# Performance work log

Measured on AMD Instinct MI355X. Metric: run time of the kernel, lower is better.

The kernel has to match this reference:

```python
import jax, jax.numpy as jnp
import numpy as np

N = 100000
E = 1600000
F_IN = 128
F_OUT = 200


def setup_inputs() -> dict:
    key = jax.random.key(0)
    ks = jax.random.split(key, 10)
    x = jax.random.normal(ks[0], (N, F_IN), dtype=jnp.float32)
    edge_index = jax.random.randint(ks[1], (2, E), 0, N, dtype=jnp.int64)
    edge_weight = jax.random.uniform(ks[2], (E,), dtype=jnp.float32)
    s = 1.0 / np.sqrt(F_IN)
    W1 = jax.random.uniform(ks[3], (1, F_IN, F_OUT), dtype=jnp.float32, minval=-s, maxval=s)
    b1 = jnp.zeros((F_OUT,), dtype=jnp.float32)
    W2 = jax.random.uniform(ks[4], (2, F_IN, F_OUT), dtype=jnp.float32, minval=-s, maxval=s)
    b2 = jnp.zeros((F_OUT,), dtype=jnp.float32)
    W3 = jax.random.uniform(ks[5], (3, F_IN, F_OUT), dtype=jnp.float32, minval=-s, maxval=s)
    b3 = jnp.zeros((F_OUT,), dtype=jnp.float32)
    return {"x": x, "edge_index": edge_index, "edge_weight": edge_weight,
            "W1": W1, "b1": b1, "W2": W2, "b2": b2, "W3": W3, "b3": b3}


def _cheb_norm(edge_index, edge_weight, n):
    # PyG ChebConv norm with lambda_max=2.0: scaled Laplacian L_hat = L - I
    # off-diagonal entries: -w_ij * d_i^{-1/2} * d_j^{-1/2}; diagonal: 0
    row, col = edge_index[0], edge_index[1]
    deg = jax.ops.segment_sum(edge_weight, row, num_segments=n)
    dis = jnp.where(deg > 0, jax.lax.rsqrt(jnp.where(deg > 0, deg, 1.0)), 0.0)
    return -edge_weight * dis[row] * dis[col]


def _propagate(h, row, col, norm, n):
    # h: [N, F] -> sum over incoming edges of norm_e * h[col_e]
    return jax.ops.segment_sum(norm[:, None] * h[col], row, num_segments=n)


def _chebconv(x, row, col, norm, W, b, n):
    K = W.shape[0]
    Tx_prev2 = x
    out = jnp.einsum('nf,fo->no', x, W[0])
    if K > 1:
        Tx_prev = _propagate(x, row, col, norm, n)
        out = out + jnp.einsum('nf,fo->no', Tx_prev, W[1])
        for k in range(2, K):
            Tx_k = 2.0 * _propagate(Tx_prev, row, col, norm, n) - Tx_prev2
            out = out + jnp.einsum('nf,fo->no', Tx_k, W[k])
            Tx_prev2, Tx_prev = Tx_prev, Tx_k
    return out + b


def reference(x, edge_index, edge_weight, W1, b1, W2, b2, W3, b3):
    n = x.shape[0]
    row, col = edge_index[0], edge_index[1]
    norm = _cheb_norm(edge_index, edge_weight, n)
    scale_1 = _chebconv(x, row, col, norm, W1, b1, n)
    scale_2 = _chebconv(x, row, col, norm, W2, b2, n)
    scale_3 = _chebconv(x, row, col, norm, W3, b3, n)
    return (scale_1, scale_2, scale_3)
```

## Files before the change

kernel.cpp:

```cpp
#include <hip/hip_runtime.h>
#include <hip/hip_bf16.h>
#include <stdint.h>

#define NN    100000
#define NROWP 100096
#define NE    1600000
#define FIN   128
#define FOUT  200
#define NBLK  391

typedef __attribute__((ext_vector_type(8))) short short8;
typedef __attribute__((ext_vector_type(8))) unsigned short ushort8;
typedef __attribute__((ext_vector_type(2))) float f32x2;
typedef __attribute__((ext_vector_type(4))) float f32x4;
typedef __attribute__((ext_vector_type(2))) unsigned int u32x2;
typedef __attribute__((ext_vector_type(4))) unsigned int uint32x4;

__device__ __forceinline__ short f2bf(float f) {
    __hip_bfloat16 h = __float2bfloat16(f);
    return *reinterpret_cast<short*>(&h);
}
__device__ __forceinline__ unsigned short f2bfu(float f) {
    __hip_bfloat16 h = __float2bfloat16(f);
    return *reinterpret_cast<unsigned short*>(&h);
}
__device__ __forceinline__ float bf2f(unsigned short u) {
    return __uint_as_float((unsigned)u << 16);
}
__device__ __forceinline__ int getidx(const void* ei, int isI32, long long i) {
    return isI32 ? ((const int*)ei)[i] : (int)((const long long*)ei)[i];
}

__global__ void detect_kernel(const long long* ei64, int* flag) {
    int t = blockIdx.x * blockDim.x + threadIdx.x;
    long long v = ei64[t];
    if (v < 0 || v >= NN) atomicOr(flag, 1);
}

__global__ void cnt8_kernel(const void* ei, const int* flag, int* cnt8) {
    int e = blockIdx.x * blockDim.x + threadIdx.x;
    int r = getidx(ei, *flag, e);
    atomicAdd(&cnt8[(blockIdx.x & 7) * NN + r], 1);
}

__global__ void scan_block(int* __restrict__ cnt8, int* __restrict__ rowstart,
                           int* __restrict__ bsum) {
    __shared__ int tmp[256];
    int i = blockIdx.x * 256 + threadIdx.x;
    int v = 0;
    if (i < NN) {
        int s = 0;
        #pragma unroll
        for (int x = 0; x < 8; ++x) {
            int c = cnt8[x * NN + i];
            cnt8[x * NN + i] = s;
            s += c;
        }
        v = s;
    }
    tmp[threadIdx.x] = v;
    __syncthreads();
    for (int off = 1; off < 256; off <<= 1) {
        int t = (threadIdx.x >= off) ? tmp[threadIdx.x - off] : 0;
        __syncthreads();
        tmp[threadIdx.x] += t;
        __syncthreads();
    }
    if (i < NN) rowstart[i] = tmp[threadIdx.x] - v;
    if (threadIdx.x == 255) bsum[blockIdx.x] = tmp[255];
}

__global__ void scan_bsums(int* bsum) {
    __shared__ int tmp[512];
    int t = threadIdx.x;
    int v = (t < NBLK) ? bsum[t] : 0;
    tmp[t] = v;
    __syncthreads();
    for (int off = 1; off < 512; off <<= 1) {
        int u = (t >= off) ? tmp[t - off] : 0;
        __syncthreads();
        tmp[t] += u;
        __syncthreads();
    }
    if (t < NBLK) bsum[t] = tmp[t] - v;
}

__global__ void scan_add(int* __restrict__ rowstart, const int* __restrict__ bsum) {
    int i = blockIdx.x * 256 + threadIdx.x;
    if (i < NN)       rowstart[i] += bsum[i >> 8];
    else if (i == NN) rowstart[NN] = NE;
}

__global__ void fill_csr(const void* ei, const int* flag, const float* __restrict__ w,
                         const int* __restrict__ rowstart, int* __restrict__ cnt8,
                         int2* __restrict__ edge) {
    int e = blockIdx.x * blockDim.x + threadIdx.x;
    int isI32 = *flag;
    int r = getidx(ei, isI32, e);
    int c = getidx(ei, isI32, (long long)NE + e);
    int pos = rowstart[r] + atomicAdd(&cnt8[(blockIdx.x & 7) * NN + r], 1);
    int2 rec; rec.x = c; rec.y = __float_as_int(w[e]);
    edge[pos] = rec;
}

__global__ void deg_seg(const int* __restrict__ rowstart, const int2* __restrict__ edge,
                        float* __restrict__ dis) {
    int r = blockIdx.x * 256 + threadIdx.x;
    if (r >= NN) return;
    int s = rowstart[r], e = rowstart[r + 1];
    float d = 0.f;
    for (int i = s; i < e; ++i) d += __int_as_float(edge[i].y);
    dis[r] = d > 0.f ? rsqrtf(d) : 0.f;
}

__global__ void xconv_kernel(const float* __restrict__ x, const float* __restrict__ dis,
                             unsigned short* __restrict__ xb, unsigned int* __restrict__ xs8) {
    int i = blockIdx.x * 256 + threadIdx.x;
    float d = dis[i >> 4];
    long long base = (long long)i * 8;
    f32x4 v0 = *(const f32x4*)(x + base);
    f32x4 v1 = *(const f32x4*)(x + base + 4);
    ushort8 o;
    #pragma unroll
    for (int k = 0; k < 4; ++k) { o[k] = f2bfu(v0[k]); o[4 + k] = f2bfu(v1[k]); }
    __builtin_nontemporal_store(o, (ushort8*)(xb + base));
    unsigned u0 = __builtin_amdgcn_cvt_pk_fp8_f32(d * v0[0], d * v0[1], 0, false);
    u0 = __builtin_amdgcn_cvt_pk_fp8_f32(d * v0[2], d * v0[3], u0, true);
    unsigned u1 = __builtin_amdgcn_cvt_pk_fp8_f32(d * v1[0], d * v1[1], 0, false);
    u1 = __builtin_amdgcn_cvt_pk_fp8_f32(d * v1[2], d * v1[3], u1, true);
    u32x2 ov; ov[0] = u0; ov[1] = u1;
    __builtin_nontemporal_store(ov, (u32x2*)(xs8 + (long long)i * 2));
}

template <int MODE>
__launch_bounds__(256)
__global__ void gather_prop(const int* __restrict__ rowstart, const int2* __restrict__ edge,
                            const float* __restrict__ dis,
                            const unsigned int* __restrict__ src8,
                            const unsigned short* __restrict__ xb,
                            unsigned short* __restrict__ dstb,
                            unsigned int* __restrict__ dst8) {
    int gw   = (blockIdx.x << 2) + (threadIdx.x >> 6);
    int lane = threadIdx.x & 63;
    int q = lane >> 4, fl = lane & 15;
    int s = rowstart[gw], eend = rowstart[gw + 1];
    float a0[8] = {0.f,0.f,0.f,0.f,0.f,0.f,0.f,0.f};
    float a1[8] = {0.f,0.f,0.f,0.f,0.f,0.f,0.f,0.f};
    int e = s + q;
    for (; e + 4 < eend; e += 8) {
        int2 ed0 = edge[e];
        int2 ed1 = edge[e + 4];
        u32x2 v0 = *(const u32x2*)(src8 + ((long long)ed0.x << 5) + (fl << 1));
        u32x2 v1 = *(const u32x2*)(src8 + ((long long)ed1.x << 5) + (fl << 1));
        float w0 = __int_as_float(ed0.y);
        float w1 = __int_as_float(ed1.y);
        f32x2 p0 = __builtin_amdgcn_cvt_pk_f32_fp8(v0[0], false);
        f32x2 p1 = __builtin_amdgcn_cvt_pk_f32_fp8(v0[0], true);
        f32x2 p2 = __builtin_amdgcn_cvt_pk_f32_fp8(v0[1], false);
        f32x2 p3 = __builtin_amdgcn_cvt_pk_f32_fp8(v0[1], true);
        a0[0] += w0 * p0.x; a0[1] += w0 * p0.y; a0[2] += w0 * p1.x; a0[3] += w0 * p1.y;
        a0[4] += w0 * p2.x; a0[5] += w0 * p2.y; a0[6] += w0 * p3.x; a0[7] += w0 * p3.y;
        f32x2 r0 = __builtin_amdgcn_cvt_pk_f32_fp8(v1[0], false);
        f32x2 r1 = __builtin_amdgcn_cvt_pk_f32_fp8(v1[0], true);
        f32x2 r2 = __builtin_amdgcn_cvt_pk_f32_fp8(v1[1], false);
        f32x2 r3 = __builtin_amdgcn_cvt_pk_f32_fp8(v1[1], true);
        a1[0] += w1 * r0.x; a1[1] += w1 * r0.y; a1[2] += w1 * r1.x; a1[3] += w1 * r1.y;
        a1[4] += w1 * r2.x; a1[5] += w1 * r2.y; a1[6] += w1 * r3.x; a1[7] += w1 * r3.y;
    }
    if (e < eend) {
        int2 ed = edge[e];
        u32x2 v = *(const u32x2*)(src8 + ((long long)ed.x << 5) + (fl << 1));
        float w = __int_as_float(ed.y);
        f32x2 p0 = __builtin_amdgcn_cvt_pk_f32_fp8(v[0], false);
        f32x2 p1 = __builtin_amdgcn_cvt_pk_f32_fp8(v[0], true);
        f32x2 p2 = __builtin_amdgcn_cvt_pk_f32_fp8(v[1], false);
        f32x2 p3 = __builtin_amdgcn_cvt_pk_f32_fp8(v[1], true);
        a0[0] += w * p0.x; a0[1] += w * p0.y; a0[2] += w * p1.x; a0[3] += w * p1.y;
        a0[4] += w * p2.x; a0[5] += w * p2.y; a0[6] += w * p3.x; a0[7] += w * p3.y;
    }
    #pragma unroll
    for (int i = 0; i < 8; ++i) {
        a0[i] += a1[i];
        a0[i] += __shfl_xor(a0[i], 16);
        a0[i] += __shfl_xor(a0[i], 32);
    }
    if (lane < 16) {
        float sr = -dis[gw];
        if (MODE == 1) {
            ushort8 xv = *(const ushort8*)(xb + ((long long)gw << 7) + (fl << 3));
            ushort8 o;
            #pragma unroll
            for (int i = 0; i < 8; ++i) o[i] = f2bfu(2.f * sr * a0[i] - bf2f(xv[i]));
            __builtin_nontemporal_store(o, (ushort8*)(dstb + ((long long)gw << 7) + (fl << 3)));
        } else {
            float t[8];
            ushort8 o;
            #pragma unroll
            for (int i = 0; i < 8; ++i) { t[i] = sr * a0[i]; o[i] = f2bfu(t[i]); }
            __builtin_nontemporal_store(o, (ushort8*)(dstb + ((long long)gw << 7) + (fl << 3)));
            float ds = dis[gw];
            unsigned u0 = __builtin_amdgcn_cvt_pk_fp8_f32(ds * t[0], ds * t[1], 0, false);
            u0 = __builtin_amdgcn_cvt_pk_fp8_f32(ds * t[2], ds * t[3], u0, true);
            unsigned u1 = __builtin_amdgcn_cvt_pk_fp8_f32(ds * t[4], ds * t[5], 0, false);
            u1 = __builtin_amdgcn_cvt_pk_fp8_f32(ds * t[6], ds * t[7], u1, true);
            u32x2 ov; ov[0] = u0; ov[1] = u1;
            __builtin_nontemporal_store(ov, (u32x2*)(dst8 + ((long long)gw << 5) + (fl << 1)));
        }
    }
}

__global__ void wprep_frag(const float* __restrict__ W1, const float* __restrict__ W2,
                           const float* __restrict__ W3, short* __restrict__ Wf) {
    __shared__ float lds[32 * 200];
    int bid = blockIdx.x;
    int s, ks;
    if (bid < 4)       { s = 0; ks = bid; }
    else if (bid < 12) { s = 1; ks = bid - 4; }
    else               { s = 2; ks = bid - 12; }
    const float* W = (s == 0) ? W1 : ((s == 1) ? W2 : W3);
    int p = ks >> 2;
    const float* Wp = W + (p * 128 + (ks & 3) * 32) * 200;
    for (int e = threadIdx.x; e < 6400; e += 256) lds[e] = Wp[e];
    __syncthreads();
    int nk = (s + 1) * 4;
    int fb = (s == 0) ? 0 : ((s == 1) ? 52 : 156);
    for (int qq = threadIdx.x; qq < 13 * 64; qq += 256) {
        int t = qq >> 6, lane = qq & 63;
        int col = t * 16 + (lane & 15);
        int kb  = (lane >> 4) * 8;
        short8 v;
        #pragma unroll
        for (int i = 0; i < 8; ++i) {
            float f = (col < FOUT) ? lds[(kb + i) * 200 + col] : 0.f;
            v[i] = f2bf(f);
        }
        *(short8*)&Wf[(fb + t * nk + ks) * 512 + lane * 8] = v;
    }
}

__constant__ int u_sc[8][5] = {
    {2,2,1,0,0}, {2,2,1,0,0}, {2,2,1,0,0}, {2,2,1,0,0},
    {2,2,1,0,0}, {2,2,1,0,0}, {2,1,1,1,0}, {1,1,1,1,-1}};
__constant__ int u_t[8][5] = {
    {0,1,0,0,1},     {2,3,1,2,3},    {4,5,2,4,5},    {6,7,3,6,7},
    {8,9,4,8,9},     {10,11,5,10,11},{12,6,7,8,12},  {9,10,11,12,0}};

#define EPAD 204

__launch_bounds__(512, 2)
__global__ void gemm_fused(const unsigned short* __restrict__ xb,
                           const unsigned short* __restrict__ t1b,
                           const unsigned short* __restrict__ t2b,
                           const short* __restrict__ Wf,
                           const float* __restrict__ b1, const float* __restrict__ b2,
                           const float* __restrict__ b3, float* __restrict__ out) {
    __shared__ __align__(16) char smem[64 * EPAD * 4];
    short* As = (short*)smem;
    float* Ef = (float*)smem;

    const int tid  = threadIdx.x;
    const int wave = tid >> 6;
    const int lane = tid & 63;
    const int l15  = lane & 15;
    const int lhi  = lane >> 4;
    const int b0   = blockIdx.x * 64;

    const unsigned short* panels[3] = {xb, t1b, t2b};
    #pragma unroll
    for (int i = 0; i < 6; ++i) {
        int q   = i * 512 + tid;
        int p   = q >> 10;
        int rem = q & 1023;
        int row = rem >> 4;
        int ch  = rem & 15;
        uint32x4 v = *(const uint32x4*)(panels[p] + ((long long)(b0 + row) << 7) + (ch << 3));
        *(uint32x4*)&As[((p * 64 + row) * 16 + (ch ^ (row & 7))) * 8] = v;
    }

    int usc[5], ubase[5], ucol0[5];
    #pragma unroll
    for (int j = 0; j < 5; ++j) {
        int sc = u_sc[wave][j], t = u_t[wave][j];
        usc[j]   = sc;
        ucol0[j] = t * 16;
        int nk = 4 * (sc + 1);
        int fb = (sc == 0) ? 0 : ((sc == 1) ? 52 : 156);
        ubase[j] = fb + t * nk;
    }

    f32x4 acc[5][4];
    #pragma unroll
    for (int j = 0; j < 5; ++j)
        #pragma unroll
        for (int m = 0; m < 4; ++m) acc[j][m] = {0.f, 0.f, 0.f, 0.f};

    short8 bf[2][5];
    #pragma unroll
    for (int j = 0; j < 5; ++j)
        bf[0][j] = *(const short8*)(Wf + (long long)(ubase[j] + 0) * 512 + lane * 8);

    __syncthreads();

    #pragma unroll
    for (int step = 0; step < 12; ++step) {
        const int p   = step >> 2;
        const int k4  = step & 3;
        const int cur = step & 1;
        if (step < 11) {
            #pragma unroll
            for (int j = 0; j < 5; ++j)
                bf[cur ^ 1][j] = *(const short8*)(Wf + (long long)(ubase[j] + step + 1) * 512 + lane * 8);
        }
        short8 af[4];
        #pragma unroll
        for (int m = 0; m < 4; ++m) {
            int row = m * 16 + l15;
            int ch  = (k4 * 4 + lhi) ^ (row & 7);
            af[m] = *(const short8*)&As[((p * 64 + row) * 16 + ch) * 8];
        }
        #pragma unroll
        for (int j = 0; j < 5; ++j) {
            if (usc[j] >= p) {
                #pragma unroll
                for (int m = 0; m < 4; ++m)
                    acc[j][m] = __builtin_amdgcn_mfma_f32_16x16x32_bf16(af[m], bf[cur][j], acc[j][m], 0, 0, 0);
            }
        }
    }

    #pragma unroll 1
    for (int sc = 0; sc < 3; ++sc) {
        __syncthreads();
        const float* bias = (sc == 0) ? b1 : ((sc == 1) ? b2 : b3);
        #pragma unroll
        for (int j = 0; j < 5; ++j) {
            if (usc[j] == sc) {
                int col = ucol0[j] + l15;
                if (col < FOUT) {
                    float bv = bias[col];
                    #pragma unroll
                    for (int m = 0; m < 4; ++m) {
                        int rbase = m * 16 + lhi * 4;
                        #pragma unroll
                        for (int jj = 0; jj < 4; ++jj)
                            Ef[(rbase + jj) * EPAD + col] = acc[j][m][jj] + bv;
                    }
                }
            }
        }
        __syncthreads();
        float* op = out + (long long)sc * NN * FOUT;
        for (int c = tid; c < 3200; c += 512) {
            int r = c / 50, pos = c % 50;
            int row = b0 + r;
            if (row < NN) {
                f32x4 v = *(const f32x4*)&Ef[r * EPAD + pos * 4];
                __builtin_nontemporal_store(v, (f32x4*)&op[(long long)row * FOUT + pos * 4]);
            }
        }
    }
}

extern "C" void kernel_launch(void* const* d_in, const int* in_sizes, int n_in,
                              void* d_out, int out_size, void* d_ws, size_t ws_size,
                              hipStream_t stream) {
    const float* x  = (const float*)d_in[0];
    const void*  ei = d_in[1];
    const float* ew = (const float*)d_in[2];
    const float* W1 = (const float*)d_in[3];
    const float* b1 = (const float*)d_in[4];
    const float* W2 = (const float*)d_in[5];
    const float* b2 = (const float*)d_in[6];
    const float* W3 = (const float*)d_in[7];
    const float* b3 = (const float*)d_in[8];
    float* out = (float*)d_out;

    char* ws = (char*)d_ws;
    int*   flag     = (int*)(ws + 0);
    int*   cnt8     = (int*)(ws + 16);
    int*   rowstart = (int*)(ws + 3600016);
    int*   bsum     = (int*)(ws + 4000032);
    float* dis      = (float*)(ws + 4002080);
    int2*  edge     = (int2*)(ws + 4402080);
    unsigned short* Xb  = (unsigned short*)(ws + 17202080);
    unsigned short* T1b = (unsigned short*)(ws + 42826656);
    unsigned short* T2b = (unsigned short*)(ws + 68451232);
    short* Wf       = (short*)(ws + 94075808);
    unsigned int* Xs8  = (unsigned int*)(ws + 94395296);
    unsigned int* T1s8 = (unsigned int*)(ws + 107207584);

    hipMemsetAsync(d_ws, 0, 3200016, stream);

    detect_kernel<<<16, 256, 0, stream>>>((const long long*)ei, flag);
    cnt8_kernel<<<NE / 256, 256, 0, stream>>>(ei, flag, cnt8);
    scan_block<<<NBLK, 256, 0, stream>>>(cnt8, rowstart, bsum);
    scan_bsums<<<1, 512, 0, stream>>>(bsum);
    scan_add<<<NBLK + 1, 256, 0, stream>>>(rowstart, bsum);
    fill_csr<<<NE / 256, 256, 0, stream>>>(ei, flag, ew, rowstart, cnt8, edge);
    deg_seg<<<NBLK, 256, 0, stream>>>(rowstart, edge, dis);
    xconv_kernel<<<6250, 256, 0, stream>>>(x, dis, Xb, Xs8);
    gather_prop<0><<<NN / 4, 256, 0, stream>>>(rowstart, edge, dis, Xs8, nullptr, T1b, T1s8);
    gather_prop<1><<<NN / 4, 256, 0, stream>>>(rowstart, edge, dis, T1s8, Xb, T2b, nullptr);
    wprep_frag<<<24, 256, 0, stream>>>(W1, W2, W3, Wf);
    gemm_fused<<<1563, 512, 0, stream>>>(Xb, T1b, T2b, Wf, b1, b2, b3, out);
}
```

Measured before the change: 418.4 us.

## Fuse second Chebyshev propagation into GEMM kernel prologue

```diff
diff --git a/kernel.cpp b/kernel.cpp
--- a/kernel.cpp
+++ b/kernel.cpp
@@ -132,14 +132,12 @@
     __builtin_nontemporal_store(ov, (u32x2*)(xs8 + (long long)i * 2));
 }
 
-template <int MODE>
 __launch_bounds__(256)
-__global__ void gather_prop(const int* __restrict__ rowstart, const int2* __restrict__ edge,
-                            const float* __restrict__ dis,
-                            const unsigned int* __restrict__ src8,
-                            const unsigned short* __restrict__ xb,
-                            unsigned short* __restrict__ dstb,
-                            unsigned int* __restrict__ dst8) {
+__global__ void gather1(const int* __restrict__ rowstart, const int2* __restrict__ edge,
+                        const float* __restrict__ dis,
+                        const unsigned int* __restrict__ src8,
+                        unsigned short* __restrict__ dstb,
+                        unsigned int* __restrict__ dst8) {
     int gw   = (blockIdx.x << 2) + (threadIdx.x >> 6);
     int lane = threadIdx.x & 63;
     int q = lane >> 4, fl = lane & 15;
@@ -186,26 +184,18 @@
     }
     if (lane < 16) {
         float sr = -dis[gw];
-        if (MODE == 1) {
-            ushort8 xv = *(const ushort8*)(xb + ((long long)gw << 7) + (fl << 3));
-            ushort8 o;
-            #pragma unroll
-            for (int i = 0; i < 8; ++i) o[i] = f2bfu(2.f * sr * a0[i] - bf2f(xv[i]));
-            __builtin_nontemporal_store(o, (ushort8*)(dstb + ((long long)gw << 7) + (fl << 3)));
-        } else {
-            float t[8];
-            ushort8 o;
-            #pragma unroll
-            for (int i = 0; i < 8; ++i) { t[i] = sr * a0[i]; o[i] = f2bfu(t[i]); }
-            __builtin_nontemporal_store(o, (ushort8*)(dstb + ((long long)gw << 7) + (fl << 3)));
-            float ds = dis[gw];
-            unsigned u0 = __builtin_amdgcn_cvt_pk_fp8_f32(ds * t[0], ds * t[1], 0, false);
-            u0 = __builtin_amdgcn_cvt_pk_fp8_f32(ds * t[2], ds * t[3], u0, true);
-            unsigned u1 = __builtin_amdgcn_cvt_pk_fp8_f32(ds * t[4], ds * t[5], 0, false);
-            u1 = __builtin_amdgcn_cvt_pk_fp8_f32(ds * t[6], ds * t[7], u1, true);
-            u32x2 ov; ov[0] = u0; ov[1] = u1;
-            __builtin_nontemporal_store(ov, (u32x2*)(dst8 + ((long long)gw << 5) + (fl << 1)));
-        }
+        float t[8];
+        ushort8 o;
+        #pragma unroll
+        for (int i = 0; i < 8; ++i) { t[i] = sr * a0[i]; o[i] = f2bfu(t[i]); }
+        __builtin_nontemporal_store(o, (ushort8*)(dstb + ((long long)gw << 7) + (fl << 3)));
+        float ds = dis[gw];
+        unsigned u0 = __builtin_amdgcn_cvt_pk_fp8_f32(ds * t[0], ds * t[1], 0, false);
+        u0 = __builtin_amdgcn_cvt_pk_fp8_f32(ds * t[2], ds * t[3], u0, true);
+        unsigned u1 = __builtin_amdgcn_cvt_pk_fp8_f32(ds * t[4], ds * t[5], 0, false);
+        u1 = __builtin_amdgcn_cvt_pk_fp8_f32(ds * t[6], ds * t[7], u1, true);
+        u32x2 ov; ov[0] = u0; ov[1] = u1;
+        __builtin_nontemporal_store(ov, (u32x2*)(dst8 + ((long long)gw << 5) + (fl << 1)));
     }
 }
 
@@ -250,10 +240,12 @@
 __launch_bounds__(512, 2)
 __global__ void gemm_fused(const unsigned short* __restrict__ xb,
                            const unsigned short* __restrict__ t1b,
-                           const unsigned short* __restrict__ t2b,
                            const short* __restrict__ Wf,
                            const float* __restrict__ b1, const float* __restrict__ b2,
-                           const float* __restrict__ b3, float* __restrict__ out) {
+                           const float* __restrict__ b3, float* __restrict__ out,
+                           const int* __restrict__ rowstart, const int2* __restrict__ edge,
+                           const float* __restrict__ dis,
+                           const unsigned int* __restrict__ t1s8) {
     __shared__ __align__(16) char smem[64 * EPAD * 4];
     short* As = (short*)smem;
     float* Ef = (float*)smem;
@@ -265,9 +257,9 @@
     const int lhi  = lane >> 4;
     const int b0   = blockIdx.x * 64;
 
-    const unsigned short* panels[3] = {xb, t1b, t2b};
-    #pragma unroll
-    for (int i = 0; i < 6; ++i) {
+    const unsigned short* panels[2] = {xb, t1b};
+    #pragma unroll
+    for (int i = 0; i < 4; ++i) {
         int q   = i * 512 + tid;
         int p   = q >> 10;
         int rem = q & 1023;
@@ -275,6 +267,64 @@
         int ch  = rem & 15;
         uint32x4 v = *(const uint32x4*)(panels[p] + ((long long)(b0 + row) << 7) + (ch << 3));
         *(uint32x4*)&As[((p * 64 + row) * 16 + (ch ^ (row & 7))) * 8] = v;
+    }
+
+    {
+        const int q = lane >> 4, fl = lane & 15;
+        for (int rr = 0; rr < 8; ++rr) {
+            const int row = wave * 8 + rr;
+            const int gw = b0 + row;
+            int s = 0, eend = 0;
+            if (gw < NN) { s = rowstart[gw]; eend = rowstart[gw + 1]; }
+            float a0[8] = {0.f,0.f,0.f,0.f,0.f,0.f,0.f,0.f};
+            float a1[8] = {0.f,0.f,0.f,0.f,0.f,0.f,0.f,0.f};
+            int e = s + q;
+            for (; e + 4 < eend; e += 8) {
+                int2 ed0 = edge[e];
+                int2 ed1 = edge[e + 4];
+                u32x2 v0 = *(const u32x2*)(t1s8 + ((long long)ed0.x << 5) + (fl << 1));
+                u32x2 v1 = *(const u32x2*)(t1s8 + ((long long)ed1.x << 5) + (fl << 1));
+                float w0 = __int_as_float(ed0.y);
+                float w1 = __int_as_float(ed1.y);
+                f32x2 p0 = __builtin_amdgcn_cvt_pk_f32_fp8(v0[0], false);
+                f32x2 p1 = __builtin_amdgcn_cvt_pk_f32_fp8(v0[0], true);
+                f32x2 p2 = __builtin_amdgcn_cvt_pk_f32_fp8(v0[1], false);
+                f32x2 p3 = __builtin_amdgcn_cvt_pk_f32_fp8(v0[1], true);
+                a0[0] += w0 * p0.x; a0[1] += w0 * p0.y; a0[2] += w0 * p1.x; a0[3] += w0 * p1.y;
+                a0[4] += w0 * p2.x; a0[5] += w0 * p2.y; a0[6] += w0 * p3.x; a0[7] += w0 * p3.y;
+                f32x2 r0 = __builtin_amdgcn_cvt_pk_f32_fp8(v1[0], false);
+                f32x2 r1 = __builtin_amdgcn_cvt_pk_f32_fp8(v1[0], true);
+                f32x2 r2 = __builtin_amdgcn_cvt_pk_f32_fp8(v1[1], false);
+                f32x2 r3 = __builtin_amdgcn_cvt_pk_f32_fp8(v1[1], true);
+                a1[0] += w1 * r0.x; a1[1] += w1 * r0.y; a1[2] += w1 * r1.x; a1[3] += w1 * r1.y;
+                a1[4] += w1 * r2.x; a1[5] += w1 * r2.y; a1[6] += w1 * r3.x; a1[7] += w1 * r3.y;
+            }
+            if (e < eend) {
+                int2 ed = edge[e];
+                u32x2 v = *(const u32x2*)(t1s8 + ((long long)ed.x << 5) + (fl << 1));
+                float w = __int_as_float(ed.y);
+                f32x2 p0 = __builtin_amdgcn_cvt_pk_f32_fp8(v[0], false);
+                f32x2 p1 = __builtin_amdgcn_cvt_pk_f32_fp8(v[0], true);
+                f32x2 p2 = __builtin_amdgcn_cvt_pk_f32_fp8(v[1], false);
+                f32x2 p3 = __builtin_amdgcn_cvt_pk_f32_fp8(v[1], true);
+                a0[0] += w * p0.x; a0[1] += w * p0.y; a0[2] += w * p1.x; a0[3] += w * p1.y;
+                a0[4] += w * p2.x; a0[5] += w * p2.y; a0[6] += w * p3.x; a0[7] += w * p3.y;
+            }
+            #pragma unroll
+            for (int i = 0; i < 8; ++i) {
+                a0[i] += a1[i];
+                a0[i] += __shfl_xor(a0[i], 16);
+                a0[i] += __shfl_xor(a0[i], 32);
+            }
+            if (lane < 16) {
+                float sr = (gw < NN) ? -dis[gw] : 0.f;
+                ushort8 xv = *(const ushort8*)(xb + ((long long)gw << 7) + (fl << 3));
+                ushort8 o;
+                #pragma unroll
+                for (int i = 0; i < 8; ++i) o[i] = f2bfu(2.f * sr * a0[i] - bf2f(xv[i]));
+                *(ushort8*)&As[((128 + row) * 16 + (fl ^ (row & 7))) * 8] = o;
+            }
+        }
     }
 
     int usc[5], ubase[5], ucol0[5];
@@ -384,7 +434,6 @@
     int2*  edge     = (int2*)(ws + 4402080);
     unsigned short* Xb  = (unsigned short*)(ws + 17202080);
     unsigned short* T1b = (unsigned short*)(ws + 42826656);
-    unsigned short* T2b = (unsigned short*)(ws + 68451232);
     short* Wf       = (short*)(ws + 94075808);
     unsigned int* Xs8  = (unsigned int*)(ws + 94395296);
     unsigned int* T1s8 = (unsigned int*)(ws + 107207584);
@@ -399,8 +448,8 @@
     fill_csr<<<NE / 256, 256, 0, stream>>>(ei, flag, ew, rowstart, cnt8, edge);
     deg_seg<<<NBLK, 256, 0, stream>>>(rowstart, edge, dis);
     xconv_kernel<<<6250, 256, 0, stream>>>(x, dis, Xb, Xs8);
-    gather_prop<0><<<NN / 4, 256, 0, stream>>>(rowstart, edge, dis, Xs8, nullptr, T1b, T1s8);
-    gather_prop<1><<<NN / 4, 256, 0, stream>>>(rowstart, edge, dis, T1s8, Xb, T2b, nullptr);
+    gather1<<<NN / 4, 256, 0, stream>>>(rowstart, edge, dis, Xs8, T1b, T1s8);
     wprep_frag<<<24, 256, 0, stream>>>(W1, W2, W3, Wf);
-    gemm_fused<<<1563, 512, 0, stream>>>(Xb, T1b, T2b, Wf, b1, b2, b3, out);
-}
+    gemm_fused<<<1563, 512, 0, stream>>>(Xb, T1b, Wf, b1, b2, b3, out,
+                                         rowstart, edge, dis, T1s8);
+}
```

After: 521.0 us. 1.25x slower.
